# Optimization experiments

Measured on AMD Instinct MI355X. Metric: run time of the kernel, lower is better.

The kernel has to match this reference:

```python
import jax, jax.numpy as jnp
import numpy as np


def setup_inputs() -> dict:
    key = jax.random.key(0)
    kq, kk, kv = jax.random.split(key, 3)
    shape = (2, 12, 4096, 64)  # [B, H, S, d]
    Q = jax.random.normal(kq, shape, dtype=jnp.float32)
    K = jax.random.normal(kk, shape, dtype=jnp.float32)
    V = jax.random.normal(kv, shape, dtype=jnp.float32)
    return {"Q": Q, "K": K, "V": V}


def reference(Q, K, V):
    d_k = K.shape[-1]
    scale = 1.0 / jnp.sqrt(jnp.asarray(d_k, dtype=Q.dtype))
    # [B,H,S,S] attention scores
    scores = jnp.einsum('bhqd,bhkd->bhqk', Q, K) * scale
    attn = jax.nn.softmax(scores, axis=-1)
    out = jnp.einsum('bhqk,bhkd->bhqd', attn, V)
    return out
```

## Files before the change

### kernel.cpp

```cpp
#include <hip/hip_runtime.h>


constexpr int Sseq = 4096;
constexpr int Dh   = 64;
constexpr int BM   = 128;
constexpr int BN   = 64;
constexpr int NT   = Sseq / BN;
constexpr float SHIFT = 10.0f;

typedef short bf16x8 __attribute__((ext_vector_type(8)));
typedef float f32x4  __attribute__((ext_vector_type(4)));

__device__ __forceinline__ unsigned short f2bf(float x) {
    union { float f; unsigned int u; } v; v.f = x;
    unsigned int r = v.u + 0x7fffu + ((v.u >> 16) & 1u);
    return (unsigned short)(r >> 16);
}

#if __has_builtin(__builtin_amdgcn_exp2f)
#define EXP2(x) __builtin_amdgcn_exp2f(x)
#else
#define EXP2(x) exp2f(x)
#endif

__device__ __forceinline__ int swz(int row, int blk8) {
    return row * 8 + (blk8 ^ (row & 7));
}

__device__ __forceinline__ void gld16(const void* g, void* l) {
    __builtin_amdgcn_global_load_lds(
        (const __attribute__((address_space(1))) void*)g,
        (__attribute__((address_space(3))) void*)l, 16, 0, 0);
}

__global__ __launch_bounds__(256)
void preconv_kernel(const float* __restrict__ K, const float* __restrict__ V,
                    unsigned short* __restrict__ ws)
{
    __shared__ unsigned short tile[8192];
    unsigned short* tK = tile;
    unsigned short* tV = tile + 4096;

    const int kb = blockIdx.x, bh = blockIdx.y, tid = threadIdx.x;
    const float4* k4 = reinterpret_cast<const float4*>(K + ((size_t)bh * Sseq + kb * BN) * Dh);
    const float4* v4 = reinterpret_cast<const float4*>(V + ((size_t)bh * Sseq + kb * BN) * Dh);
    unsigned short* kimg = ws + (size_t)(bh * NT + kb) * 8192;

    float4 kv[4], vv[4];
    #pragma unroll
    for (int it = 0; it < 4; ++it) kv[it] = k4[it * 256 + tid];
    #pragma unroll
    for (int it = 0; it < 4; ++it) vv[it] = v4[it * 256 + tid];

    #pragma unroll
    for (int it = 0; it < 4; ++it) {
        const int f  = it * 256 + tid;
        const int r  = f >> 4;
        const int c4 = (f & 15) * 4;
        const int pr = (r & 32) | ((r & 4) << 2) | ((r & 24) >> 1) | (r & 3);
        unsigned int lo32 = (unsigned int)f2bf(kv[it].x) | ((unsigned int)f2bf(kv[it].y) << 16);
        unsigned int hi32 = (unsigned int)f2bf(kv[it].z) | ((unsigned int)f2bf(kv[it].w) << 16);
        *reinterpret_cast<uint2*>(&tK[swz(pr, c4 >> 3) * 8 + (c4 & 7)]) = make_uint2(lo32, hi32);
        tV[swz(c4 + 0, r >> 3) * 8 + (r & 7)] = f2bf(vv[it].x);
        tV[swz(c4 + 1, r >> 3) * 8 + (r & 7)] = f2bf(vv[it].y);
        tV[swz(c4 + 2, r >> 3) * 8 + (r & 7)] = f2bf(vv[it].z);
        tV[swz(c4 + 3, r >> 3) * 8 + (r & 7)] = f2bf(vv[it].w);
    }
    __syncthreads();

    const uint4* src = reinterpret_cast<const uint4*>(tile);
    uint4* dst = reinterpret_cast<uint4*>(kimg);
    #pragma unroll
    for (int i = 0; i < 4; ++i)
        dst[i * 256 + tid] = src[i * 256 + tid];
}

__global__ __launch_bounds__(256, 3)
void fattn_kernel(const float* __restrict__ Q, const unsigned short* __restrict__ ws,
                  float* __restrict__ O)
{
    __shared__ unsigned short sKV[2][8192];

    const int tid  = threadIdx.x;
    const int wave = tid >> 6;
    const int lane = tid & 63;
    const int lo   = lane & 15;
    const int quad = lane >> 4;

    const int qblk = blockIdx.x;
    const int bh   = blockIdx.y;

    const float* gQ = Q + (size_t)bh * Sseq * Dh;
    float*       gO = O + (size_t)bh * Sseq * Dh;

    const float qscale = 0.18033688011112042f;
    bf16x8 qf[2][2];
    #pragma unroll
    for (int u = 0; u < 2; ++u) {
        const int qrow = qblk * BM + wave * 32 + u * 16 + lo;
        const float* qp = gQ + (size_t)qrow * Dh + quad * 8;
        #pragma unroll
        for (int c = 0; c < 2; ++c) {
            float4 a = *reinterpret_cast<const float4*>(qp + c * 32);
            float4 b = *reinterpret_cast<const float4*>(qp + c * 32 + 4);
            qf[u][c][0] = (short)f2bf(a.x * qscale);
            qf[u][c][1] = (short)f2bf(a.y * qscale);
            qf[u][c][2] = (short)f2bf(a.z * qscale);
            qf[u][c][3] = (short)f2bf(a.w * qscale);
            qf[u][c][4] = (short)f2bf(b.x * qscale);
            qf[u][c][5] = (short)f2bf(b.y * qscale);
            qf[u][c][6] = (short)f2bf(b.z * qscale);
            qf[u][c][7] = (short)f2bf(b.w * qscale);
        }
    }

    bf16x8 onesb = (bf16x8)0;
    if (lo == 0) {
        #pragma unroll
        for (int j = 0; j < 8; ++j) onesb[j] = (short)0x3F80;
    }

    f32x4 accv[2][4];
    f32x4 acc5[2];
    #pragma unroll
    for (int u = 0; u < 2; ++u) {
        acc5[u] = f32x4{0.f, 0.f, 0.f, 0.f};
        #pragma unroll
        for (int t = 0; t < 4; ++t) accv[u][t] = f32x4{0.f, 0.f, 0.f, 0.f};
    }

    union AFrag { unsigned int w[4]; bf16x8 b; };

    const char* img = (const char*)(ws + (size_t)bh * NT * 8192);
    const int ubase = wave * 1024;
    const int goff  = ubase + lane * 16;

    {
        char* dst = (char*)sKV[0];
        gld16(img + goff,          dst + ubase);
        gld16(img + 4096  + goff,  dst + 4096  + ubase);
        gld16(img + 8192  + goff,  dst + 8192  + ubase);
        gld16(img + 12288 + goff,  dst + 12288 + ubase);
    }
    __syncthreads();

    for (int kb = 0; kb < NT; ++kb) {
        const int buf = kb & 1;
        const unsigned short* sK  = sKV[buf];
        const unsigned short* sVt = sKV[buf] + 4096;

        if (kb + 1 < NT) {
            const char* nimg = img + (size_t)(kb + 1) * 16384;
            char* dst = (char*)sKV[buf ^ 1];
            gld16(nimg + goff,          dst + ubase);
            gld16(nimg + 4096  + goff,  dst + 4096  + ubase);
            gld16(nimg + 8192  + goff,  dst + 8192  + ubase);
            gld16(nimg + 12288 + goff,  dst + 12288 + ubase);
        }

        AFrag af[2][2];
        #pragma unroll
        for (int t = 0; t < 4; ++t) {
            const bf16x8 k0 = *reinterpret_cast<const bf16x8*>(&sK[swz(16 * t + lo, quad) * 8]);
            const bf16x8 k1 = *reinterpret_cast<const bf16x8*>(&sK[swz(16 * t + lo, 4 + quad) * 8]);
            #pragma unroll
            for (int u = 0; u < 2; ++u) {
                f32x4 s = f32x4{-SHIFT, -SHIFT, -SHIFT, -SHIFT};
                s = __builtin_amdgcn_mfma_f32_16x16x32_bf16(k0, qf[u][0], s, 0, 0, 0);
                s = __builtin_amdgcn_mfma_f32_16x16x32_bf16(k1, qf[u][1], s, 0, 0, 0);
                af[u][t >> 1].w[2 * (t & 1) + 0] =
                    (unsigned int)f2bf(EXP2(s[0])) | ((unsigned int)f2bf(EXP2(s[1])) << 16);
                af[u][t >> 1].w[2 * (t & 1) + 1] =
                    (unsigned int)f2bf(EXP2(s[2])) | ((unsigned int)f2bf(EXP2(s[3])) << 16);
            }
        }

        __builtin_amdgcn_s_setprio(1);
        #pragma unroll
        for (int c = 0; c < 2; ++c) {
            #pragma unroll
            for (int u = 0; u < 2; ++u)
                acc5[u] = __builtin_amdgcn_mfma_f32_16x16x32_bf16(af[u][c].b, onesb, acc5[u], 0, 0, 0);
            #pragma unroll
            for (int t2 = 0; t2 < 4; ++t2) {
                const bf16x8 vf = *reinterpret_cast<const bf16x8*>(&sVt[swz(16 * t2 + lo, 4 * c + quad) * 8]);
                #pragma unroll
                for (int u = 0; u < 2; ++u)
                    accv[u][t2] = __builtin_amdgcn_mfma_f32_16x16x32_bf16(af[u][c].b, vf, accv[u][t2], 0, 0, 0);
            }
        }
        __builtin_amdgcn_s_setprio(0);

        __syncthreads();
    }

    #pragma unroll
    for (int u = 0; u < 2; ++u) {
        const int qbase = qblk * BM + wave * 32 + u * 16 + quad * 4;
        #pragma unroll
        for (int r = 0; r < 4; ++r) {
            const float ls  = __shfl(acc5[u][r], (lane & 48));
            const float inv = 1.0f / ls;
            float* op = gO + (size_t)(qbase + r) * Dh;
            #pragma unroll
            for (int t2 = 0; t2 < 4; ++t2)
                op[t2 * 16 + lo] = accv[u][t2][r] * inv;
        }
    }
}

constexpr int LD = 72;
__global__ __launch_bounds__(256, 2)
void fattn_fallback(const float* __restrict__ Q, const float* __restrict__ K,
                    const float* __restrict__ V, float* __restrict__ O)
{
    __shared__ unsigned short sK [BN * LD];
    __shared__ unsigned short sVt[Dh * LD];
    __shared__ unsigned short sP [4 * 16 * LD];

    const int tid  = threadIdx.x;
    const int wave = tid >> 6;
    const int lane = tid & 63;
    const int lo   = lane & 15;
    const int quad = lane >> 4;
    const int qblk = blockIdx.x;
    const int bh   = blockIdx.y;

    const float* gQ = Q + (size_t)bh * Sseq * Dh;
    const float* gK = K + (size_t)bh * Sseq * Dh;
    const float* gV = V + (size_t)bh * Sseq * Dh;
    float*       gO = O + (size_t)bh * Sseq * Dh;

    const float qscale = 0.18033688011112042f;
    bf16x8 qf[2];
    {
        const int qrow = qblk * 64 + wave * 16 + lo;
        const float* qp = gQ + (size_t)qrow * Dh + quad * 8;
        #pragma unroll
        for (int c = 0; c < 2; ++c) {
            float4 a = *reinterpret_cast<const float4*>(qp + c * 32);
            float4 b = *reinterpret_cast<const float4*>(qp + c * 32 + 4);
            qf[c][0] = (short)f2bf(a.x * qscale); qf[c][1] = (short)f2bf(a.y * qscale);
            qf[c][2] = (short)f2bf(a.z * qscale); qf[c][3] = (short)f2bf(a.w * qscale);
            qf[c][4] = (short)f2bf(b.x * qscale); qf[c][5] = (short)f2bf(b.y * qscale);
            qf[c][6] = (short)f2bf(b.z * qscale); qf[c][7] = (short)f2bf(b.w * qscale);
        }
    }

    float m_prev[4] = {-1e30f, -1e30f, -1e30f, -1e30f};
    float lsum[4]   = {0.f, 0.f, 0.f, 0.f};
    f32x4 accv[4];
    #pragma unroll
    for (int t = 0; t < 4; ++t) accv[t] = f32x4{0.f, 0.f, 0.f, 0.f};
    unsigned short* sPw = &sP[wave * 16 * LD];

    for (int kb = 0; kb < Sseq / BN; ++kb) {
        const float4* k4 = reinterpret_cast<const float4*>(gK + (size_t)kb * BN * Dh);
        const float4* v4 = reinterpret_cast<const float4*>(gV + (size_t)kb * BN * Dh);
        #pragma unroll
        for (int it = 0; it < 4; ++it) {
            const int f   = it * 256 + tid;
            const int row = f >> 4;
            const int c4  = (f & 15) * 4;
            float4 kv = k4[f];
            unsigned int lo32 = (unsigned int)f2bf(kv.x) | ((unsigned int)f2bf(kv.y) << 16);
            unsigned int hi32 = (unsigned int)f2bf(kv.z) | ((unsigned int)f2bf(kv.w) << 16);
            *reinterpret_cast<uint2*>(&sK[row * LD + c4]) = make_uint2(lo32, hi32);
            float4 vv = v4[f];
            sVt[(c4 + 0) * LD + row] = f2bf(vv.x);
            sVt[(c4 + 1) * LD + row] = f2bf(vv.y);
            sVt[(c4 + 2) * LD + row] = f2bf(vv.z);
            sVt[(c4 + 3) * LD + row] = f2bf(vv.w);
        }
        __syncthreads();

        float sc[4][4];
        #pragma unroll
        for (int t = 0; t < 4; ++t) {
            const bf16x8 k0 = *reinterpret_cast<const bf16x8*>(&sK[(t * 16 + lo) * LD + 0  + quad * 8]);
            const bf16x8 k1 = *reinterpret_cast<const bf16x8*>(&sK[(t * 16 + lo) * LD + 32 + quad * 8]);
            f32x4 s = f32x4{0.f, 0.f, 0.f, 0.f};
            s = __builtin_amdgcn_mfma_f32_16x16x32_bf16(qf[0], k0, s, 0, 0, 0);
            s = __builtin_amdgcn_mfma_f32_16x16x32_bf16(qf[1], k1, s, 0, 0, 0);
            sc[t][0] = s[0]; sc[t][1] = s[1]; sc[t][2] = s[2]; sc[t][3] = s[3];
        }

        float bm[4];
        #pragma unroll
        for (int r = 0; r < 4; ++r)
            bm[r] = fmaxf(fmaxf(sc[0][r], sc[1][r]), fmaxf(sc[2][r], sc[3][r]));
        #pragma unroll
        for (int m = 1; m <= 8; m <<= 1) {
            #pragma unroll
            for (int r = 0; r < 4; ++r) bm[r] = fmaxf(bm[r], __shfl_xor(bm[r], m));
        }
        float m_new[4], alpha[4];
        #pragma unroll
        for (int r = 0; r < 4; ++r) {
            m_new[r] = fmaxf(m_prev[r], bm[r]);
            alpha[r] = exp2f(m_prev[r] - m_new[r]);
            m_prev[r] = m_new[r];
        }
        float ps[4][4];
        float rs[4] = {0.f, 0.f, 0.f, 0.f};
        #pragma unroll
        for (int t = 0; t < 4; ++t) {
            #pragma unroll
            for (int r = 0; r < 4; ++r) { ps[t][r] = exp2f(sc[t][r] - m_new[r]); rs[r] += ps[t][r]; }
        }
        #pragma unroll
        for (int m = 1; m <= 8; m <<= 1) {
            #pragma unroll
            for (int r = 0; r < 4; ++r) rs[r] += __shfl_xor(rs[r], m);
        }
        #pragma unroll
        for (int r = 0; r < 4; ++r) lsum[r] = lsum[r] * alpha[r] + rs[r];
        #pragma unroll
        for (int t = 0; t < 4; ++t) {
            #pragma unroll
            for (int r = 0; r < 4; ++r) accv[t][r] *= alpha[r];
        }
        #pragma unroll
        for (int t = 0; t < 4; ++t) {
            #pragma unroll
            for (int r = 0; r < 4; ++r)
                sPw[(quad * 4 + r) * LD + t * 16 + lo] = f2bf(ps[t][r]);
        }
        #pragma unroll
        for (int c = 0; c < 2; ++c) {
            const bf16x8 af = *reinterpret_cast<const bf16x8*>(&sPw[lo * LD + c * 32 + quad * 8]);
            #pragma unroll
            for (int t2 = 0; t2 < 4; ++t2) {
                const bf16x8 vf = *reinterpret_cast<const bf16x8*>(&sVt[(t2 * 16 + lo) * LD + c * 32 + quad * 8]);
                accv[t2] = __builtin_amdgcn_mfma_f32_16x16x32_bf16(af, vf, accv[t2], 0, 0, 0);
            }
        }
        __syncthreads();
    }

    const int qbase = qblk * 64 + wave * 16 + quad * 4;
    #pragma unroll
    for (int r = 0; r < 4; ++r) {
        const float inv = 1.0f / lsum[r];
        float* op = gO + (size_t)(qbase + r) * Dh;
        #pragma unroll
        for (int t2 = 0; t2 < 4; ++t2)
            op[t2 * 16 + lo] = accv[t2][r] * inv;
    }
}

extern "C" void kernel_launch(void* const* d_in, const int* in_sizes, int n_in,
                              void* d_out, int out_size, void* d_ws, size_t ws_size,
                              hipStream_t stream) {
    const float* Q = (const float*)d_in[0];
    const float* K = (const float*)d_in[1];
    const float* V = (const float*)d_in[2];
    float* O = (float*)d_out;
    const int BH = in_sizes[0] / (Sseq * Dh);
    const size_t ws_needed = (size_t)BH * NT * 16384;
    if (ws_size >= ws_needed) {
        preconv_kernel<<<dim3(NT, BH), 256, 0, stream>>>(K, V, (unsigned short*)d_ws);
        fattn_kernel<<<dim3(Sseq / BM, BH), 256, 0, stream>>>(Q, (const unsigned short*)d_ws, O);
    } else {
        fattn_fallback<<<dim3(Sseq / 64, BH), 256, 0, stream>>>(Q, K, V, O);
    }
}
```

Measured before the change: 228.1 us.

## Fuse K/V preconversion and attention into one cooperative kernel with grid sync

The K/V bf16 preconversion and the flash-attention kernel are merged into one cooperative launch. Each block first builds two K/V tile images in workspace, then all blocks meet at a grid-wide barrier before running the attention body. This removes the second kernel launch and the gap between the two kernels. In exchange it adds a grid sync and needs all 768 blocks to be resident at once; if the cooperative launch fails, the code falls back to the two-kernel path.

```diff
diff --git a/kernel.cpp b/kernel.cpp
--- a/kernel.cpp
+++ b/kernel.cpp
@@ -1,4 +1,7 @@
 #include <hip/hip_runtime.h>
+#include <hip/hip_cooperative_groups.h>
+
+namespace cg = cooperative_groups;
 
 
 constexpr int Sseq = 4096;
@@ -33,18 +36,15 @@
         (__attribute__((address_space(3))) void*)l, 16, 0, 0);
 }
 
-__global__ __launch_bounds__(256)
-void preconv_kernel(const float* __restrict__ K, const float* __restrict__ V,
-                    unsigned short* __restrict__ ws)
-{
-    __shared__ unsigned short tile[8192];
-    unsigned short* tK = tile;
-    unsigned short* tV = tile + 4096;
-
-    const int kb = blockIdx.x, bh = blockIdx.y, tid = threadIdx.x;
-    const float4* k4 = reinterpret_cast<const float4*>(K + ((size_t)bh * Sseq + kb * BN) * Dh);
-    const float4* v4 = reinterpret_cast<const float4*>(V + ((size_t)bh * Sseq + kb * BN) * Dh);
-    unsigned short* kimg = ws + (size_t)(bh * NT + kb) * 8192;
+__device__ __forceinline__ void build_tile_image(
+    const float* __restrict__ K, const float* __restrict__ V,
+    unsigned short* __restrict__ ws, unsigned short* __restrict__ stage ,
+    int tbh, int tkb, int tid)
+{
+    unsigned short* tK = stage;
+    unsigned short* tV = stage + 4096;
+    const float4* k4 = reinterpret_cast<const float4*>(K + ((size_t)tbh * Sseq + tkb * BN) * Dh);
+    const float4* v4 = reinterpret_cast<const float4*>(V + ((size_t)tbh * Sseq + tkb * BN) * Dh);
 
     float4 kv[4], vv[4];
     #pragma unroll
@@ -68,19 +68,18 @@
     }
     __syncthreads();
 
-    const uint4* src = reinterpret_cast<const uint4*>(tile);
-    uint4* dst = reinterpret_cast<uint4*>(kimg);
+    const uint4* src = reinterpret_cast<const uint4*>(stage);
+    uint4* dst = reinterpret_cast<uint4*>(ws + (size_t)(tbh * NT + tkb) * 8192);
     #pragma unroll
     for (int i = 0; i < 4; ++i)
         dst[i * 256 + tid] = src[i * 256 + tid];
-}
-
-__global__ __launch_bounds__(256, 3)
-void fattn_kernel(const float* __restrict__ Q, const unsigned short* __restrict__ ws,
-                  float* __restrict__ O)
-{
-    __shared__ unsigned short sKV[2][8192];
-
+    __syncthreads();
+}
+
+__device__ __forceinline__ void fattn_body(
+    const float* __restrict__ Q, const unsigned short* __restrict__ ws,
+    float* __restrict__ O, unsigned short (*sKV)[8192])
+{
     const int tid  = threadIdx.x;
     const int wave = tid >> 6;
     const int lane = tid & 63;
@@ -207,6 +206,46 @@
                 op[t2 * 16 + lo] = accv[u][t2][r] * inv;
         }
     }
+}
+
+__global__ __launch_bounds__(256, 3)
+void fused_attn_kernel(const float* __restrict__ Q, const float* __restrict__ K,
+                       const float* __restrict__ V, unsigned short* __restrict__ ws,
+                       float* __restrict__ O)
+{
+    __shared__ unsigned short sKV[2][8192];
+    const int tid = threadIdx.x;
+
+    {
+        const int lb = blockIdx.y * gridDim.x + blockIdx.x;
+        #pragma unroll
+        for (int s = 0; s < 2; ++s) {
+            const int T = 2 * lb + s;
+            build_tile_image(K, V, ws, sKV[0], T >> 6, T & 63, tid);
+        }
+    }
+
+    __threadfence();
+    cg::this_grid().sync();
+    __threadfence();
+
+    fattn_body(Q, ws, O, sKV);
+}
+
+__global__ __launch_bounds__(256)
+void preconv_kernel(const float* __restrict__ K, const float* __restrict__ V,
+                    unsigned short* __restrict__ ws)
+{
+    __shared__ unsigned short tile[8192];
+    build_tile_image(K, V, ws, tile, blockIdx.y, blockIdx.x, threadIdx.x);
+}
+
+__global__ __launch_bounds__(256, 3)
+void fattn_kernel(const float* __restrict__ Q, const unsigned short* __restrict__ ws,
+                  float* __restrict__ O)
+{
+    __shared__ unsigned short sKV[2][8192];
+    fattn_body(Q, ws, O, sKV);
 }
 
 constexpr int LD = 72;
@@ -359,8 +398,16 @@
     const int BH = in_sizes[0] / (Sseq * Dh);
     const size_t ws_needed = (size_t)BH * NT * 16384;
     if (ws_size >= ws_needed) {
-        preconv_kernel<<<dim3(NT, BH), 256, 0, stream>>>(K, V, (unsigned short*)d_ws);
-        fattn_kernel<<<dim3(Sseq / BM, BH), 256, 0, stream>>>(Q, (const unsigned short*)d_ws, O);
+        unsigned short* wsp = (unsigned short*)d_ws;
+        const float* Kp = K; const float* Vp = V; const float* Qp = Q; float* Op = O;
+        void* args[] = { (void*)&Qp, (void*)&Kp, (void*)&Vp, (void*)&wsp, (void*)&Op };
+        hipError_t e = hipLaunchCooperativeKernel(
+            (const void*)fused_attn_kernel, dim3(Sseq / BM, BH), dim3(256),
+            args, 0, stream);
+        if (e != hipSuccess) {
+            preconv_kernel<<<dim3(NT, BH), 256, 0, stream>>>(K, V, wsp);
+            fattn_kernel<<<dim3(Sseq / BM, BH), 256, 0, stream>>>(Q, wsp, O);
+        }
     } else {
         fattn_fallback<<<dim3(Sseq / 64, BH), 256, 0, stream>>>(Q, K, V, O);
     }
```

Result: slower. 453.8 us (+99.0%).
